# Performance work log

Measured on AMD Instinct MI355X. Metric: run time of the kernel, lower is better.

## Reference

```python
import jax, jax.numpy as jnp
import numpy as np

IN_F, OUT_F = 1024, 1024
GRID_SIZE, SPLINE_ORDER = 5, 3
BATCH = 4096
GRID_LO, GRID_HI = -1.0, 1.0


def _make_grid():
    h = (GRID_HI - GRID_LO) / GRID_SIZE
    g = jnp.arange(-SPLINE_ORDER, GRID_SIZE + SPLINE_ORDER + 1, dtype=jnp.float32) * h + GRID_LO  # [12]
    return jnp.broadcast_to(g, (IN_F, g.shape[0]))  # [in, 12]


def setup_inputs() -> dict:
    key = jax.random.key(0)
    k1, k2, k3 = jax.random.split(key, 3)
    x = jax.random.normal(k1, (BATCH, IN_F), dtype=jnp.float32)
    base_weight = jax.random.normal(k2, (OUT_F, IN_F), dtype=jnp.float32) * (1.0 / np.sqrt(IN_F))
    spline_weight = jax.random.normal(k3, (OUT_F, IN_F, GRID_SIZE + SPLINE_ORDER), dtype=jnp.float32) * 0.1
    spline_scaler = jnp.ones((OUT_F, IN_F), dtype=jnp.float32)
    grid = _make_grid()
    return {"x": x, "base_weight": base_weight, "spline_weight": spline_weight,
            "spline_scaler": spline_scaler, "grid": grid}


def b_splines(x, grid):
    # x: [B, in], grid: [in, 12] -> bases: [B, in, grid_size+spline_order]
    xe = x[..., None]  # [B, in, 1]
    bases = ((xe >= grid[:, :-1]) & (xe < grid[:, 1:])).astype(x.dtype)  # [B, in, 11]
    for k in range(1, SPLINE_ORDER + 1):
        t0 = grid[:, :-(k + 1)]
        t1 = grid[:, k:-1]
        t2 = grid[:, k + 1:]
        t3 = grid[:, 1:-k]
        bases = ((xe - t0) / (t1 - t0 + 1e-8) * bases[..., :-1]
                 + (t2 - xe) / (t2 - t3 + 1e-8) * bases[..., 1:])
    return bases


def reference(x, base_weight, spline_weight, spline_scaler, grid):
    base_output = jax.nn.silu(x) @ base_weight.T  # [B, out]
    spline_basis = b_splines(x, grid)             # [B, in, 8]
    spline_output = jnp.einsum('bij,oij,oi->bo', spline_basis, spline_weight, spline_scaler)
    return base_output + spline_output
```

## Files before the change

kernel.cpp:

```cpp
#include <hip/hip_runtime.h>
#include <hip/hip_bf16.h>
#include <stdint.h>
#include <stddef.h>

#define IN_F     1024
#define OUT_F    1024
#define BATCH    4096
#define NSPLINE  8
#define KDIM     (IN_F * 9)
#define GRIDPTS  12

typedef __bf16 bf16;
typedef __bf16 bf16x2 __attribute__((ext_vector_type(2)));
typedef __bf16 bf16x8 __attribute__((ext_vector_type(8)));
typedef float  f32x4  __attribute__((ext_vector_type(4)));

#define NB_BUILD (BATCH * IN_F / 512)
#define NB_PACK  (OUT_F * IN_F / 512)

__global__ __launch_bounds__(256) void prep(const float* __restrict__ x,
                                            const float* __restrict__ grid,
                                            const float* __restrict__ bw,
                                            const float* __restrict__ sw,
                                            const float* __restrict__ sc,
                                            bf16* __restrict__ A,
                                            bf16* __restrict__ W)
{
    __shared__ float g[GRIDPTS];
    __shared__ float rec[33];

    if (blockIdx.x < NB_BUILD) {
        if (threadIdx.x < GRIDPTS) g[threadIdx.x] = grid[threadIdx.x];
        __syncthreads();
        if (threadIdx.x < 33) {
            const int k = threadIdx.x / 11 + 1;
            const int j = threadIdx.x % 11;
            if (j + k <= 11) rec[threadIdx.x] = 1.0f / (g[j + k] - g[j] + 1e-8f);
        }
        __syncthreads();

        const int idx2 = blockIdx.x * 256 + threadIdx.x;
        const int e0 = idx2 * 2;
        const int b = e0 >> 10;
        const int i = e0 & 1023;
        const float2 xv2 = *(const float2*)(x + e0);

        float bs[2][11];
#pragma unroll
        for (int u = 0; u < 2; ++u) {
            const float xv = u ? xv2.y : xv2.x;
#pragma unroll
            for (int j = 0; j < 11; ++j)
                bs[u][j] = (xv >= g[j] && xv < g[j + 1]) ? 1.0f : 0.0f;
#pragma unroll
            for (int k = 1; k <= 3; ++k) {
                const float* rk = &rec[(k - 1) * 11];
#pragma unroll
                for (int j = 0; j < 10; ++j) {
                    if (j <= 10 - k) {
                        bs[u][j] = (xv - g[j]) * rk[j] * bs[u][j]
                                 + (g[j + k + 1] - xv) * rk[j + 1] * bs[u][j + 1];
                    }
                }
            }
        }

        const float s0 = xv2.x / (1.0f + __expf(-xv2.x));
        const float s1 = xv2.y / (1.0f + __expf(-xv2.y));

        bf16* rowp = A + (size_t)b * KDIM;
        *(bf16x2*)&rowp[i] = (bf16x2){(bf16)s0, (bf16)s1};
#pragma unroll
        for (int j = 0; j < NSPLINE; ++j)
            *(bf16x2*)&rowp[(size_t)(j + 1) * IN_F + i] =
                (bf16x2){(bf16)bs[0][j], (bf16)bs[1][j]};
    } else {
        const int idx2 = (blockIdx.x - NB_BUILD) * 256 + threadIdx.x;
        const int e0 = idx2 * 2;
        const int i = e0 & 1023;
        const float2 s2 = *(const float2*)(sc + e0);
        const float2 bw2 = *(const float2*)(bw + e0);

        bf16* rowp = W + (size_t)(e0 >> 10) * KDIM;
        *(bf16x2*)&rowp[i] = (bf16x2){(bf16)bw2.x, (bf16)bw2.y};

        const float4* swv = (const float4*)(sw + (size_t)e0 * NSPLINE);
        const float4 a0 = swv[0], a1 = swv[1];
        const float4 c0 = swv[2], c1 = swv[3];
        float w0[NSPLINE] = {a0.x, a0.y, a0.z, a0.w, a1.x, a1.y, a1.z, a1.w};
        float w1[NSPLINE] = {c0.x, c0.y, c0.z, c0.w, c1.x, c1.y, c1.z, c1.w};
#pragma unroll
        for (int j = 0; j < NSPLINE; ++j)
            *(bf16x2*)&rowp[(size_t)(j + 1) * IN_F + i] =
                (bf16x2){(bf16)(w0[j] * s2.x), (bf16)(w1[j] * s2.y)};
    }
}

#define BM8 256
#define BN8 256
#define BK8 64
#define SPLIT 4

#define GLOAD_LDS16(gp, lp)                                                          \
    __builtin_amdgcn_global_load_lds((const __attribute__((address_space(1))) void*)(gp), \
                                     (__attribute__((address_space(3))) void*)(lp), 16, 0, 0)

__global__ __launch_bounds__(512, 2) void gemm8(const bf16* __restrict__ A,
                                                const bf16* __restrict__ B,
                                                float* __restrict__ C,
                                                int kLen)
{
    __shared__ bf16 lds[8 * 8192];

    const int tid  = threadIdx.x;
    const int wave = tid >> 6;
    const int lane = tid & 63;

    const int nwg  = gridDim.x;
    const int q    = nwg >> 3;
    const int wgid = (blockIdx.x & 7) * q + (blockIdx.x >> 3);
    const int nxy  = (BATCH / BM8) * (OUT_F / BN8);
    const int z    = wgid / nxy;
    const int rem  = wgid - z * nxy;
    const int by   = rem >> 4;
    const int bx   = rem & 15;

    const int bm   = bx * BM8;
    const int bcol = by * BN8;
    const int kBase = z * kLen;
    C += (size_t)z * BATCH * OUT_F;

    const int wr = (wave >> 2) * 128;
    const int wc = (wave & 3) * 64;

    f32x4 acc[8][4] = {};

    const int NT   = kLen / BK8;
    const int hmax = 4 * NT;

    const int srow = tid >> 2;
    const int sch  = (((tid & 3) ^ ((tid >> 3) & 3))) * 8;
    const bf16* baseA = A + (size_t)(bm + srow) * KDIM + kBase + sch;
    const bf16* baseB = B + (size_t)(bcol + srow) * KDIM + kBase + sch;
    const size_t rstep = (size_t)128 * KDIM;
    bf16* ldsw = &lds[wave * 512];

    auto stage = [&](int h) {
        if (h < hmax) {
            const int t   = h >> 2;
            const int th  = h & 3;
            const int kof = t * BK8 + ((th >> 1) ? 32 : 0);
            const bf16* src = (th & 1) ? baseB : baseA;
            bf16* l0 = ldsw + (h & 7) * 8192;
            GLOAD_LDS16(src + kof, l0);
            GLOAD_LDS16(src + kof + rstep, l0 + 4096);
        }
    };

    for (int h = 0; h < 6; ++h) stage(h);
    asm volatile("s_waitcnt vmcnt(4)" ::: "memory");
    __builtin_amdgcn_s_barrier();

    const int rowk = lane & 15;
    const int kc   = lane >> 4;
    const int kxor = (kc ^ ((rowk >> 1) & 3)) * 8;

#define LDSFRAG(slot, row) (*(const bf16x8*)&lds[(slot) * 8192 + (row) * 32 + kxor])

    bf16x8 a[4], b[4], a2[4], b2[4];
#pragma unroll
    for (int m = 0; m < 4; ++m) a[m] = LDSFRAG(0, wr + m * 16 + rowk);
#pragma unroll
    for (int n = 0; n < 4; ++n) b[n] = LDSFRAG(1, wc + n * 16 + rowk);

    for (int t = 0; t < NT; ++t) {
        const int h0  = 4 * t;
        const int sA0 = (h0 + 0) & 7;
        const int sA1 = (h0 + 2) & 7, sB1 = (h0 + 3) & 7;

        stage(h0 + 6);
#pragma unroll
        for (int m = 0; m < 4; ++m) a2[m] = LDSFRAG(sA0, wr + 64 + m * 16 + rowk);
        __builtin_amdgcn_sched_barrier(0);
        __builtin_amdgcn_s_setprio(1);
#pragma unroll
        for (int m = 0; m < 4; ++m)
#pragma unroll
            for (int n = 0; n < 4; ++n)
                acc[m][n] = __builtin_amdgcn_mfma_f32_16x16x32_bf16(a[m], b[n], acc[m][n], 0, 0, 0);
        __builtin_amdgcn_s_setprio(0);
        __builtin_amdgcn_s_barrier();

        stage(h0 + 7);
#pragma unroll
        for (int m = 0; m < 4; ++m) a[m] = LDSFRAG(sA1, wr + m * 16 + rowk);
#pragma unroll
        for (int n = 0; n < 4; ++n) b2[n] = LDSFRAG(sB1, wc + n * 16 + rowk);
        __builtin_amdgcn_sched_barrier(0);
        __builtin_amdgcn_s_setprio(1);
#pragma unroll
        for (int m = 0; m < 4; ++m)
#pragma unroll
            for (int n = 0; n < 4; ++n)
                acc[4 + m][n] = __builtin_amdgcn_mfma_f32_16x16x32_bf16(a2[m], b[n], acc[4 + m][n], 0, 0, 0);
        __builtin_amdgcn_s_setprio(0);
        __builtin_amdgcn_s_barrier();

        stage(h0 + 8);
#pragma unroll
        for (int m = 0; m < 4; ++m) a2[m] = LDSFRAG(sA1, wr + 64 + m * 16 + rowk);
        __builtin_amdgcn_sched_barrier(0);
        __builtin_amdgcn_s_setprio(1);
#pragma unroll
        for (int m = 0; m < 4; ++m)
#pragma unroll
            for (int n = 0; n < 4; ++n)
                acc[m][n] = __builtin_amdgcn_mfma_f32_16x16x32_bf16(a[m], b2[n], acc[m][n], 0, 0, 0);
        __builtin_amdgcn_s_setprio(0);
        __builtin_amdgcn_s_barrier();

        stage(h0 + 9);
        __builtin_amdgcn_sched_barrier(0);
        __builtin_amdgcn_s_setprio(1);
#pragma unroll
        for (int m = 0; m < 4; ++m)
#pragma unroll
            for (int n = 0; n < 4; ++n)
                acc[4 + m][n] = __builtin_amdgcn_mfma_f32_16x16x32_bf16(a2[m], b2[n], acc[4 + m][n], 0, 0, 0);
        __builtin_amdgcn_s_setprio(0);
        if (t < NT - 2)       asm volatile("s_waitcnt vmcnt(4)" ::: "memory");
        else if (t == NT - 2) asm volatile("s_waitcnt vmcnt(0)" ::: "memory");
        if (t + 1 < NT) {
            const int nA0 = (h0 + 4) & 7, nB0 = (h0 + 5) & 7;
#pragma unroll
            for (int m = 0; m < 4; ++m) a[m] = LDSFRAG(nA0, wr + m * 16 + rowk);
#pragma unroll
            for (int n = 0; n < 4; ++n) b[n] = LDSFRAG(nB0, wc + n * 16 + rowk);
        }
        __builtin_amdgcn_s_barrier();
    }
#undef LDSFRAG

    const int ccol = lane & 15;
    const int crow = (lane >> 4) * 4;
#pragma unroll
    for (int mf = 0; mf < 8; ++mf) {
#pragma unroll
        for (int nf = 0; nf < 4; ++nf) {
            float* cp = C + (size_t)(bm + wr + mf * 16 + crow) * OUT_F + (bcol + wc + nf * 16 + ccol);
#pragma unroll
            for (int r = 0; r < 4; ++r)
                cp[(size_t)r * OUT_F] = acc[mf][nf][r];
        }
    }
}

__global__ __launch_bounds__(256) void reduce_partials(const float4* __restrict__ P,
                                                       float4* __restrict__ out,
                                                       int n4)
{
    const int stride = gridDim.x * 256;
    for (int i = blockIdx.x * 256 + threadIdx.x; i < n4; i += stride) {
        float4 s = P[i];
#pragma unroll
        for (int p = 1; p < SPLIT; ++p) {
            const float4 q = P[(size_t)p * n4 + i];
            s.x += q.x; s.y += q.y; s.z += q.z; s.w += q.w;
        }
        out[i] = s;
    }
}

extern "C" void kernel_launch(void* const* d_in, const int* in_sizes, int n_in,
                              void* d_out, int out_size, void* d_ws, size_t ws_size,
                              hipStream_t stream)
{
    const float* x  = (const float*)d_in[0];
    const float* bw = (const float*)d_in[1];
    const float* sw = (const float*)d_in[2];
    const float* sc = (const float*)d_in[3];
    const float* gr = (const float*)d_in[4];
    float* out = (float*)d_out;

    bf16* A = (bf16*)d_ws;
    bf16* W = A + (size_t)BATCH * KDIM;
    float* parts = (float*)(W + (size_t)OUT_F * KDIM);

    prep<<<NB_BUILD + NB_PACK, 256, 0, stream>>>(x, gr, bw, sw, sc, A, W);

    const int nblk = (BATCH / BM8) * (OUT_F / BN8) * SPLIT;
    gemm8<<<nblk, 512, 0, stream>>>(A, W, parts, KDIM / SPLIT);

    const int n4 = BATCH * OUT_F / 4;
    reduce_partials<<<2048, 256, 0, stream>>>((const float4*)parts, (float4*)out, n4);
}
```

Before: 121.1 us.

## Shrink GEMM tile to 256x128x32 with simple double buffering and higher occupancy

Replaces the 256x256x64 tile and its eight-slot, four-phase LDS ring with a 256x128 tile, BK=32 and a plain two-stage double buffer that waits for all loads each iteration. Launch bounds move to 4 blocks per CU, LDS drops to 48KB, and K length becomes a compile-time constant. The aim is to rely on more resident workgroups to hide latency instead of the deep software pipeline. The cost is lower arithmetic intensity, more global and L2 traffic per FLOP, and a full vmcnt(0) stall every K step.

```diff
diff --git a/kernel.cpp b/kernel.cpp
--- a/kernel.cpp
+++ b/kernel.cpp
@@ -97,20 +97,21 @@
 }
 
 #define BM8 256
-#define BN8 256
-#define BK8 64
+#define BN8 128
+#define BK8 32
 #define SPLIT 4
+#define KLEN (KDIM / SPLIT)
+#define NT8  (KLEN / BK8)
 
 #define GLOAD_LDS16(gp, lp)                                                          \
     __builtin_amdgcn_global_load_lds((const __attribute__((address_space(1))) void*)(gp), \
                                      (__attribute__((address_space(3))) void*)(lp), 16, 0, 0)
 
-__global__ __launch_bounds__(512, 2) void gemm8(const bf16* __restrict__ A,
+__global__ __launch_bounds__(512, 4) void gemm8(const bf16* __restrict__ A,
                                                 const bf16* __restrict__ B,
-                                                float* __restrict__ C,
-                                                int kLen)
-{
-    __shared__ bf16 lds[8 * 8192];
+                                                float* __restrict__ C)
+{
+    __shared__ bf16 lds[24576];
 
     const int tid  = threadIdx.x;
     const int wave = tid >> 6;
@@ -127,126 +128,82 @@
 
     const int bm   = bx * BM8;
     const int bcol = by * BN8;
-    const int kBase = z * kLen;
+    const int kBase = z * KLEN;
     C += (size_t)z * BATCH * OUT_F;
 
     const int wr = (wave >> 2) * 128;
-    const int wc = (wave & 3) * 64;
-
-    f32x4 acc[8][4] = {};
-
-    const int NT   = kLen / BK8;
-    const int hmax = 4 * NT;
+    const int wc = (wave & 3) * 32;
+
+    f32x4 acc[8][2] = {};
 
     const int srow = tid >> 2;
     const int sch  = (((tid & 3) ^ ((tid >> 3) & 3))) * 8;
-    const bf16* baseA = A + (size_t)(bm + srow) * KDIM + kBase + sch;
-    const bf16* baseB = B + (size_t)(bcol + srow) * KDIM + kBase + sch;
-    const size_t rstep = (size_t)128 * KDIM;
-    bf16* ldsw = &lds[wave * 512];
-
-    auto stage = [&](int h) {
-        if (h < hmax) {
-            const int t   = h >> 2;
-            const int th  = h & 3;
-            const int kof = t * BK8 + ((th >> 1) ? 32 : 0);
-            const bf16* src = (th & 1) ? baseB : baseA;
-            bf16* l0 = ldsw + (h & 7) * 8192;
-            GLOAD_LDS16(src + kof, l0);
-            GLOAD_LDS16(src + kof + rstep, l0 + 4096);
-        }
+    const bf16* pA0 = A + (size_t)(bm + srow) * KDIM + kBase + sch;
+    const bf16* pA1 = pA0 + (size_t)128 * KDIM;
+    const bf16* pB0 = B + (size_t)(bcol + srow) * KDIM + kBase + sch;
+    bf16* ldswA = lds + wave * 512;
+    bf16* ldswB = lds + 16384 + wave * 512;
+
+    auto stageA = [&](int t, int s) {
+        const int kof = t * BK8;
+        GLOAD_LDS16(pA0 + kof, ldswA + s * 8192);
+        GLOAD_LDS16(pA1 + kof, ldswA + s * 8192 + 4096);
     };
-
-    for (int h = 0; h < 6; ++h) stage(h);
-    asm volatile("s_waitcnt vmcnt(4)" ::: "memory");
+    auto stageB = [&](int t, int s) {
+        GLOAD_LDS16(pB0 + t * BK8, ldswB + s * 4096);
+    };
+
+    stageA(0, 0);
+    stageB(0, 0);
+    asm volatile("s_waitcnt vmcnt(0)" ::: "memory");
     __builtin_amdgcn_s_barrier();
 
     const int rowk = lane & 15;
     const int kc   = lane >> 4;
     const int kxor = (kc ^ ((rowk >> 1) & 3)) * 8;
 
-#define LDSFRAG(slot, row) (*(const bf16x8*)&lds[(slot) * 8192 + (row) * 32 + kxor])
-
-    bf16x8 a[4], b[4], a2[4], b2[4];
-#pragma unroll
-    for (int m = 0; m < 4; ++m) a[m] = LDSFRAG(0, wr + m * 16 + rowk);
-#pragma unroll
-    for (int n = 0; n < 4; ++n) b[n] = LDSFRAG(1, wc + n * 16 + rowk);
-
-    for (int t = 0; t < NT; ++t) {
-        const int h0  = 4 * t;
-        const int sA0 = (h0 + 0) & 7;
-        const int sA1 = (h0 + 2) & 7, sB1 = (h0 + 3) & 7;
-
-        stage(h0 + 6);
-#pragma unroll
-        for (int m = 0; m < 4; ++m) a2[m] = LDSFRAG(sA0, wr + 64 + m * 16 + rowk);
+#define LDSA(s, row) (*(const bf16x8*)&lds[(s) * 8192 + (row) * 32 + kxor])
+#define LDSB(s, row) (*(const bf16x8*)&lds[16384 + (s) * 4096 + (row) * 32 + kxor])
+
+    for (int t = 0; t < NT8; ++t) {
+        const int p = t & 1;
+        bf16x8 a[4], b[2], a2[4];
+
+        if (t + 1 < NT8) stageA(t + 1, 1 - p);
+#pragma unroll
+        for (int m = 0; m < 4; ++m) a[m] = LDSA(p, wr + m * 16 + rowk);
+#pragma unroll
+        for (int n = 0; n < 2; ++n) b[n] = LDSB(p, wc + n * 16 + rowk);
+        if (t + 1 < NT8) stageB(t + 1, 1 - p);
+#pragma unroll
+        for (int m = 0; m < 4; ++m) a2[m] = LDSA(p, wr + 64 + m * 16 + rowk);
         __builtin_amdgcn_sched_barrier(0);
+
         __builtin_amdgcn_s_setprio(1);
 #pragma unroll
         for (int m = 0; m < 4; ++m)
 #pragma unroll
-            for (int n = 0; n < 4; ++n)
+            for (int n = 0; n < 2; ++n)
                 acc[m][n] = __builtin_amdgcn_mfma_f32_16x16x32_bf16(a[m], b[n], acc[m][n], 0, 0, 0);
-        __builtin_amdgcn_s_setprio(0);
-        __builtin_amdgcn_s_barrier();
-
-        stage(h0 + 7);
-#pragma unroll
-        for (int m = 0; m < 4; ++m) a[m] = LDSFRAG(sA1, wr + m * 16 + rowk);
-#pragma unroll
-        for (int n = 0; n < 4; ++n) b2[n] = LDSFRAG(sB1, wc + n * 16 + rowk);
-        __builtin_amdgcn_sched_barrier(0);
-        __builtin_amdgcn_s_setprio(1);
 #pragma unroll
         for (int m = 0; m < 4; ++m)
 #pragma unroll
-            for (int n = 0; n < 4; ++n)
+            for (int n = 0; n < 2; ++n)
                 acc[4 + m][n] = __builtin_amdgcn_mfma_f32_16x16x32_bf16(a2[m], b[n], acc[4 + m][n], 0, 0, 0);
         __builtin_amdgcn_s_setprio(0);
+
+        if (t + 1 < NT8) asm volatile("s_waitcnt vmcnt(0)" ::: "memory");
         __builtin_amdgcn_s_barrier();
-
-        stage(h0 + 8);
-#pragma unroll
-        for (int m = 0; m < 4; ++m) a2[m] = LDSFRAG(sA1, wr + 64 + m * 16 + rowk);
-        __builtin_amdgcn_sched_barrier(0);
-        __builtin_amdgcn_s_setprio(1);
-#pragma unroll
-        for (int m = 0; m < 4; ++m)
-#pragma unroll
-            for (int n = 0; n < 4; ++n)
-                acc[m][n] = __builtin_amdgcn_mfma_f32_16x16x32_bf16(a[m], b2[n], acc[m][n], 0, 0, 0);
-        __builtin_amdgcn_s_setprio(0);
-        __builtin_amdgcn_s_barrier();
-
-        stage(h0 + 9);
-        __builtin_amdgcn_sched_barrier(0);
-        __builtin_amdgcn_s_setprio(1);
-#pragma unroll
-        for (int m = 0; m < 4; ++m)
-#pragma unroll
-            for (int n = 0; n < 4; ++n)
-                acc[4 + m][n] = __builtin_amdgcn_mfma_f32_16x16x32_bf16(a2[m], b2[n], acc[4 + m][n], 0, 0, 0);
-        __builtin_amdgcn_s_setprio(0);
-        if (t < NT - 2)       asm volatile("s_waitcnt vmcnt(4)" ::: "memory");
-        else if (t == NT - 2) asm volatile("s_waitcnt vmcnt(0)" ::: "memory");
-        if (t + 1 < NT) {
-            const int nA0 = (h0 + 4) & 7, nB0 = (h0 + 5) & 7;
-#pragma unroll
-            for (int m = 0; m < 4; ++m) a[m] = LDSFRAG(nA0, wr + m * 16 + rowk);
-#pragma unroll
-            for (int n = 0; n < 4; ++n) b[n] = LDSFRAG(nB0, wc + n * 16 + rowk);
-        }
-        __builtin_amdgcn_s_barrier();
-    }
-#undef LDSFRAG
+    }
+#undef LDSA
+#undef LDSB
 
     const int ccol = lane & 15;
     const int crow = (lane >> 4) * 4;
 #pragma unroll
     for (int mf = 0; mf < 8; ++mf) {
 #pragma unroll
-        for (int nf = 0; nf < 4; ++nf) {
+        for (int nf = 0; nf < 2; ++nf) {
             float* cp = C + (size_t)(bm + wr + mf * 16 + crow) * OUT_F + (bcol + wc + nf * 16 + ccol);
 #pragma unroll
             for (int r = 0; r < 4; ++r)
@@ -289,7 +246,7 @@
     prep<<<NB_BUILD + NB_PACK, 256, 0, stream>>>(x, gr, bw, sw, sc, A, W);
 
     const int nblk = (BATCH / BM8) * (OUT_F / BN8) * SPLIT;
-    gemm8<<<nblk, 512, 0, stream>>>(A, W, parts, KDIM / SPLIT);
+    gemm8<<<nblk, 512, 0, stream>>>(A, W, parts);
 
     const int n4 = BATCH * OUT_F / 4;
     reduce_partials<<<2048, 256, 0, stream>>>((const float4*)parts, (float4*)out, n4);
```

Result: slower. 127.7 us (+5.5%).
